# Kernel optimization log

Measured on AMD Instinct MI355X. Metric: run time of the kernel, lower is better.

Reference implementation:

```python
import jax, jax.numpy as jnp
import numpy as np

G = 8          # GroupNorm groups
EPS = 1e-5
L = 4          # num_layers
C = 64         # hidden_channels
CIN = 2        # in_channels


def group_norm(x, gamma, beta):
    B, Cc, H, W = x.shape
    xr = x.reshape(B, G, Cc // G, H, W)
    mu = xr.mean(axis=(2, 3, 4), keepdims=True)
    var = xr.var(axis=(2, 3, 4), keepdims=True)
    xn = ((xr - mu) * jax.lax.rsqrt(var + EPS)).reshape(B, Cc, H, W)
    return xn * gamma[:, None, None] + beta[:, None, None]


def conv1x1(x, w, b):
    # x: [B,Ci,H,W], w: [Co,Ci] -> [B,Co,H,W]
    return jnp.einsum('bchw,oc->bohw', x, w) + b[None, :, None, None]


def conv3x3(x, w, b):
    y = jax.lax.conv_general_dilated(x, w, (1, 1), 'SAME',
                                     dimension_numbers=('NCHW', 'OIHW', 'NCHW'))
    return y + b[None, :, None, None]


def setup_inputs() -> dict:
    key = jax.random.key(0)
    ks = jax.random.split(key, 20)
    s = 0.05
    inp = {
        'x': jax.random.normal(ks[0], (2, CIN, 256, 256), jnp.float32),
        'hidden': jnp.zeros((2, L, C, C), jnp.float32),
        'W_in': jax.random.normal(ks[1], (C, CIN, 3, 3), jnp.float32) * s,
        'b_in': jnp.zeros((C,), jnp.float32),
        'gamma': jnp.ones((L, C), jnp.float32),
        'beta': jnp.zeros((L, C), jnp.float32),
        'Wq': jax.random.normal(ks[2], (L, C, C), jnp.float32) * s,
        'bq': jnp.zeros((L, C), jnp.float32),
        'Wk': jax.random.normal(ks[3], (L, C, C), jnp.float32) * s,
        'bk': jnp.zeros((L, C), jnp.float32),
        'Wv': jax.random.normal(ks[4], (L, C, C), jnp.float32) * s,
        'bv': jnp.zeros((L, C), jnp.float32),
        'Wg': jax.random.normal(ks[5], (L, 2 * C, C), jnp.float32) * s,
        'bg': jnp.zeros((L, 2 * C), jnp.float32),
        'Wp': jax.random.normal(ks[6], (L, C, C), jnp.float32) * s,
        'bp': jnp.zeros((L, C), jnp.float32),
        'W_out': jax.random.normal(ks[7], (CIN, C, 3, 3), jnp.float32) * s,
        'b_out': jnp.zeros((CIN,), jnp.float32),
    }
    return inp


def gla_layer(feat, prev_mem, gamma, beta, Wq, bq, Wk, bk, Wv, bv, Wg, bg, Wp, bp):
    B, Cc, H, W = feat.shape
    N = H * W
    scale = Cc ** (-0.5)
    xn = group_norm(feat, gamma, beta)
    q = conv1x1(xn, Wq, bq).reshape(B, Cc, N) * scale
    k = conv1x1(xn, Wk, bk).reshape(B, Cc, N)
    v = conv1x1(xn, Wv, bv).reshape(B, Cc, N)
    gates = conv1x1(xn, Wg, bg).reshape(B, 2 * Cc, N)
    f_gate = jax.nn.sigmoid(gates[:, :Cc])
    i_gate = jax.nn.sigmoid(gates[:, Cc:])
    k_gated = k * i_gate
    new_knowledge = jnp.einsum('bcn,bdn->bcd', k_gated, v) / N  # [B,C,C]
    global_forget = f_gate.mean(axis=2)[:, :, None]              # [B,C,1]
    new_mem = global_forget * prev_mem + new_knowledge
    retrieved = jnp.einsum('bcn,bcd->bdn', q, new_mem).reshape(B, Cc, H, W)
    out = conv1x1(retrieved, Wp, bp) + feat
    return out, new_mem


def reference(x, hidden, W_in, b_in, gamma, beta, Wq, bq, Wk, bk, Wv, bv,
              Wg, bg, Wp, bp, W_out, b_out):
    feat = conv3x3(x, W_in, b_in)
    mems = []
    for i in range(L):
        feat, m = gla_layer(feat, hidden[:, i], gamma[i], beta[i],
                            Wq[i], bq[i], Wk[i], bk[i], Wv[i], bv[i],
                            Wg[i], bg[i], Wp[i], bp[i])
        mems.append(m)
    new_hidden = jnp.stack(mems, axis=1)  # [B,L,C,C]
    out = conv3x3(feat, W_out, b_out) + x
    return out, new_hidden
```

## Files before the change

kernel.cpp:

```cpp
#include <hip/hip_runtime.h>
#include <hip/hip_bf16.h>

typedef __hip_bfloat16 bf16;
typedef __attribute__((ext_vector_type(8))) short bf16x8;
typedef __attribute__((ext_vector_type(4))) short short4v;
typedef __attribute__((ext_vector_type(4))) float f32x4;

#define BATCH 2
#define CH 64
#define NPIX 65536
#define HDIM 256
#define NLAYER 4
#define NGRP 8

#define OFS_FEAT   0ull
#define OFS_KNOW   33554432ull
#define OFS_FSUM   33685504ull
#define OFS_SSUM   33701888ull
#define OFS_BEFF   33718272ull
#define OFS_MEFFB  33718784ull
#define OFS_WKB    33735168ull
#define OFS_WVB    33767936ull
#define OFS_WGB    33800704ull
#define OFS_WTOUT  33866240ull
#define OFS_WPB    33870848ull
#define OFS_WQTB   33903616ull
#define ZERO_BYTES 163840

__device__ __forceinline__ float sigmoidf_(float x){ return 1.0f/(1.0f+__expf(-x)); }

__device__ __forceinline__ short f2bs(float x){
  unsigned u = __float_as_uint(x);
  u += 0x7fffu + ((u >> 16) & 1u);
  return (short)(u >> 16);
}

__device__ __forceinline__ float waveReduce(float v){
  #pragma unroll
  for (int off=32; off; off>>=1) v += __shfl_xor(v, off, 64);
  return v;
}

__global__ void k_prepw(const float* __restrict__ Wk, const float* __restrict__ Wv,
                        const float* __restrict__ Wg, const float* __restrict__ Wout,
                        const float* __restrict__ Wp, const float* __restrict__ Wq,
                        short* __restrict__ Wkb, short* __restrict__ Wvb,
                        short* __restrict__ Wgb, float* __restrict__ wtout,
                        short* __restrict__ Wpb, short* __restrict__ Wqtb){
  int i = blockIdx.x*256 + threadIdx.x;
  if (i < 16384){
    Wkb[i] = f2bs(Wk[i]);
    Wvb[i] = f2bs(Wv[i]);
    Wpb[i] = f2bs(Wp[i]);
    int l = i >> 12, within = i & 4095;
    int e = within >> 6, c = within & 63;
    Wqtb[i] = f2bs(Wq[l*4096 + c*64 + e]);
  }
  if (i < 32768) Wgb[i] = f2bs(Wg[i]);
  if (i < 1152){
    int o = i / 576, rem = i % 576;
    int k = rem >> 6, c = rem & 63;
    wtout[(o*9 + k)*64 + c] = Wout[o*576 + c*9 + k];
  }
}

__device__ __forceinline__ void blockStats(const float* gs, const float* gq,
                                           float* ssum_b, int t){
  __shared__ float sacc[16];
  if (t < 16) sacc[t] = 0.f;
  __syncthreads();
  #pragma unroll
  for (int g=0; g<NGRP; g++){
    float s  = waveReduce(gs[g]);
    float sq = waveReduce(gq[g]);
    if ((t & 63) == 0){ atomicAdd(&sacc[g*2], s); atomicAdd(&sacc[g*2+1], sq); }
  }
  __syncthreads();
  if (t < 16) atomicAdd(&ssum_b[t*32], sacc[t]);
}

__global__ void k_conv_in(const float* __restrict__ x, const float* __restrict__ w,
                          const float* __restrict__ bias,
                          float* __restrict__ feat, float* __restrict__ ssum){
  int b = blockIdx.y;
  int t = threadIdx.x;
  int n = blockIdx.x*256 + t;
  int y = n >> 8, xx = n & 255;
  float patch[18];
  int idx = 0;
  #pragma unroll
  for (int ci=0; ci<2; ci++)
    #pragma unroll
    for (int dy=-1; dy<=1; dy++)
      #pragma unroll
      for (int dx=-1; dx<=1; dx++){
        int yy = y+dy, xc = xx+dx;
        float v = 0.f;
        if (yy>=0 && yy<HDIM && xc>=0 && xc<HDIM)
          v = x[((b*2+ci)*HDIM + yy)*HDIM + xc];
        patch[idx++] = v;
      }
  float gs[NGRP], gq[NGRP];
  #pragma unroll
  for (int g=0; g<NGRP; g++){ gs[g]=0.f; gq[g]=0.f; }
  float* fb = feat + ((size_t)b*NPIX + n)*64;
  #pragma unroll
  for (int c4=0; c4<16; c4++){
    f32x4 ov;
    #pragma unroll
    for (int j=0;j<4;j++){
      int o = c4*4 + j;
      float acc = bias[o];
      #pragma unroll
      for (int k=0; k<18; k++) acc += w[o*18+k]*patch[k];
      ov[j] = acc;
      gs[o>>3] += acc; gq[o>>3] += acc*acc;
    }
    *(f32x4*)(fb + c4*4) = ov;
  }
  blockStats(gs, gq, ssum + b*512, t);
}

__device__ __forceinline__ void gnCoef(const float* __restrict__ ssum_l, int b, int t,
                                       const float* __restrict__ gammaP,
                                       const float* __restrict__ betaP, int l,
                                       float* s_gnA, float* s_gnB){
  if (t < 64){
    int g = t >> 3;
    const float inv = 1.0f/(8.0f*NPIX);
    float s  = ssum_l[(b*16 + g*2)*32];
    float sq = ssum_l[(b*16 + g*2 + 1)*32];
    float mu = s*inv;
    float var = sq*inv - mu*mu;
    float rstd = rsqrtf(var + 1e-5f);
    float A = rstd * gammaP[l*64 + t];
    s_gnA[t] = A;
    s_gnB[t] = betaP[l*64 + t] - mu * A;
  }
}

__global__ __launch_bounds__(256,3) void k_qkvg_know(
    const float* __restrict__ feat, const float* __restrict__ ssum_l,
    const float* __restrict__ gammaP, const float* __restrict__ betaP,
    const short* __restrict__ Wkb, const float* __restrict__ bkP,
    const short* __restrict__ Wvb, const float* __restrict__ bvP,
    const short* __restrict__ Wgb, const float* __restrict__ bgP,
    int l, float* __restrict__ know, float* __restrict__ f_sum)
{
  int b = blockIdx.y;
  int n0 = blockIdx.x * 128;
  int rep = blockIdx.x & 3;
  int t = threadIdx.x;
  int w = t >> 6;
  int lane = t & 63;
  int m = lane & 15;
  int quad = lane >> 4;
  int rowbase = w*16;

  __shared__ short s_buf[17408];
  short* s_kg = s_buf;
  short* s_v  = s_buf + 8704;
  short* s_xn = s_buf;
  __shared__ float s_gnA[64], s_gnB[64];

  gnCoef(ssum_l, b, t, gammaP, betaP, l, s_gnA, s_gnB);

  float bkv[4], biv[4], bvv[4], bfv[4], fs[4];
  #pragma unroll
  for (int r=0;r<4;r++){
    int row = rowbase + quad*4 + r;
    bkv[r] = bkP[l*64 + row];
    biv[r] = bgP[l*128 + 64 + row];
    bvv[r] = bvP[l*64 + row];
    bfv[r] = bgP[l*128 + row];
    fs[r] = 0.f;
  }
  f32x4 z4 = {0.f,0.f,0.f,0.f};
  f32x4 accn[4];
  #pragma unroll
  for (int dt=0;dt<4;dt++) accn[dt] = z4;

  __syncthreads();

  const float* fbase = feat + ((size_t)b*NPIX + n0)*64;
  #pragma unroll
  for (int i=0;i<8;i++){
    int chunk = t + i*256;
    int px = chunk >> 4, cq = chunk & 15;
    f32x4 fv = *(const f32x4*)(fbase + px*64 + cq*4);
    short4v xs;
    #pragma unroll
    for (int j=0;j<4;j++)
      xs[j] = f2bs(fmaf(fv[j], s_gnA[cq*4+j], s_gnB[cq*4+j]));
    *(short4v*)&s_xn[px*72 + cq*4] = xs;
  }
  __syncthreads();

  bf16x8 Bf[2][8];
  #pragma unroll
  for (int kc=0;kc<2;kc++)
    #pragma unroll
    for (int nt=0;nt<8;nt++)
      Bf[kc][nt] = *(const bf16x8*)&s_xn[(nt*16+m)*72 + kc*32 + quad*8];
  __syncthreads();

  {
    bf16x8 Ak[2], Ai[2];
    #pragma unroll
    for (int kc=0;kc<2;kc++){
      Ak[kc] = *(const bf16x8*)&Wkb[l*4096 + (rowbase+m)*64 + kc*32 + quad*8];
      Ai[kc] = *(const bf16x8*)&Wgb[l*8192 + (64+rowbase+m)*64 + kc*32 + quad*8];
    }
    #pragma unroll
    for (int half=0; half<2; half++){
      f32x4 acck[4], acci[4];
      #pragma unroll
      for (int q4=0;q4<4;q4++){ acck[q4]=z4; acci[q4]=z4; }
      #pragma unroll
      for (int kc=0;kc<2;kc++)
        #pragma unroll
        for (int q4=0;q4<4;q4++){
          acck[q4] = __builtin_amdgcn_mfma_f32_16x16x32_bf16(Ak[kc], Bf[kc][half*4+q4], acck[q4], 0,0,0);
          acci[q4] = __builtin_amdgcn_mfma_f32_16x16x32_bf16(Ai[kc], Bf[kc][half*4+q4], acci[q4], 0,0,0);
        }
      #pragma unroll
      for (int q4=0;q4<4;q4++){
        int nt = half*4+q4;
        #pragma unroll
        for (int r=0;r<4;r++){
          int row = rowbase + quad*4 + r;
          float kv = acck[q4][r] + bkv[r];
          float iv = acci[q4][r] + biv[r];
          s_kg[row*136 + nt*16 + m] = f2bs(kv * sigmoidf_(iv));
        }
      }
    }
  }
  {
    bf16x8 Av[2];
    #pragma unroll
    for (int kc=0;kc<2;kc++)
      Av[kc] = *(const bf16x8*)&Wvb[l*4096 + (rowbase+m)*64 + kc*32 + quad*8];
    #pragma unroll
    for (int half=0; half<2; half++){
      f32x4 accv[4];
      #pragma unroll
      for (int q4=0;q4<4;q4++) accv[q4]=z4;
      #pragma unroll
      for (int kc=0;kc<2;kc++)
        #pragma unroll
        for (int q4=0;q4<4;q4++)
          accv[q4] = __builtin_amdgcn_mfma_f32_16x16x32_bf16(Av[kc], Bf[kc][half*4+q4], accv[q4], 0,0,0);
      #pragma unroll
      for (int q4=0;q4<4;q4++){
        int nt = half*4+q4;
        #pragma unroll
        for (int r=0;r<4;r++){
          int row = rowbase + quad*4 + r;
          s_v[row*136 + nt*16 + m] = f2bs(accv[q4][r] + bvv[r]);
        }
      }
    }
  }
  {
    bf16x8 Af[2];
    #pragma unroll
    for (int kc=0;kc<2;kc++)
      Af[kc] = *(const bf16x8*)&Wgb[l*8192 + (rowbase+m)*64 + kc*32 + quad*8];
    #pragma unroll
    for (int half=0; half<2; half++){
      f32x4 accf[4];
      #pragma unroll
      for (int q4=0;q4<4;q4++) accf[q4]=z4;
      #pragma unroll
      for (int kc=0;kc<2;kc++)
        #pragma unroll
        for (int q4=0;q4<4;q4++)
          accf[q4] = __builtin_amdgcn_mfma_f32_16x16x32_bf16(Af[kc], Bf[kc][half*4+q4], accf[q4], 0,0,0);
      #pragma unroll
      for (int q4=0;q4<4;q4++)
        #pragma unroll
        for (int r=0;r<4;r++)
          fs[r] += sigmoidf_(accf[q4][r] + bfv[r]);
    }
  }
  __syncthreads();

  #pragma unroll
  for (int kc4=0; kc4<4; kc4++){
    bf16x8 a = *(const bf16x8*)&s_kg[(rowbase + m)*136 + kc4*32 + quad*8];
    #pragma unroll
    for (int dt=0; dt<4; dt++){
      bf16x8 bv8 = *(const bf16x8*)&s_v[(dt*16 + m)*136 + kc4*32 + quad*8];
      accn[dt] = __builtin_amdgcn_mfma_f32_16x16x32_bf16(a, bv8, accn[dt], 0,0,0);
    }
  }

  #pragma unroll
  for (int off=1; off<16; off<<=1)
    #pragma unroll
    for (int r=0;r<4;r++) fs[r] += __shfl_xor(fs[r], off, 64);
  if (m == 0){
    #pragma unroll
    for (int r=0;r<4;r++)
      atomicAdd(&f_sum[(b*64 + rowbase + quad*4 + r)*32], fs[r]);
  }
  float* kr = know + (size_t)(rep*2 + b)*4096;
  #pragma unroll
  for (int dt=0;dt<4;dt++)
    #pragma unroll
    for (int r=0;r<4;r++)
      atomicAdd(&kr[(rowbase + quad*4 + r)*64 + dt*16 + m], accn[dt][r]);
}

__global__ __launch_bounds__(256) void k_memupd_meff(
    float* __restrict__ know, float* __restrict__ f_sum,
    const float* __restrict__ hidden_in,
    const short* __restrict__ Wpb, const short* __restrict__ Wqtb,
    const float* __restrict__ bqP, const float* __restrict__ bpP,
    int l, float* __restrict__ hidden_out,
    short* __restrict__ Meffb, float* __restrict__ beff,
    float* __restrict__ ssum_next)
{
  int b = blockIdx.x;
  int t = threadIdx.x;
  int w = t >> 6;
  int lane = t & 63;
  int m = lane & 15;
  int quad = lane >> 4;

  __shared__ short s_memb[64*72];
  __shared__ short s_mfb[64*72];
  __shared__ float s_bq[64];

  if (t < 64) s_bq[t] = bqP[l*64 + t];

  const float invN = 1.0f/(float)NPIX;
  #pragma unroll
  for (int i=0;i<16;i++){
    int cd = t + i*256;
    int c = cd >> 6, d = cd & 63;
    float fmean = f_sum[(b*64 + c)*32] * invN;
    float kn = 0.f;
    #pragma unroll
    for (int rep=0; rep<4; rep++){
      kn += know[(size_t)(rep*2+b)*4096 + cd];
      know[(size_t)(rep*2+b)*4096 + cd] = 0.f;
    }
    kn *= invN;
    float pm = hidden_in[(size_t)(b*NLAYER+l)*4096 + cd];
    float nm = fmean*pm + kn;
    hidden_out[(size_t)(b*NLAYER+l)*4096 + cd] = nm;
    s_memb[c*72 + d] = f2bs(nm);
  }
  __syncthreads();
  if (t < 64) f_sum[(b*64 + t)*32] = 0.f;
  if (t < 16) ssum_next[(b*16 + t)*32] = 0.f;

  f32x4 z4 = {0.f,0.f,0.f,0.f};

  bf16x8 Ap[2];
  #pragma unroll
  for (int kc=0;kc<2;kc++)
    Ap[kc] = *(const bf16x8*)&Wpb[l*4096 + (w*16+m)*64 + kc*32 + quad*8];

  float be[4];
  #pragma unroll
  for (int r=0;r<4;r++) be[r] = 0.f;

  #pragma unroll
  for (int ct=0; ct<4; ct++){
    f32x4 a = z4;
    #pragma unroll
    for (int kc=0;kc<2;kc++){
      bf16x8 Bm = *(const bf16x8*)&s_memb[(ct*16+m)*72 + kc*32 + quad*8];
      a = __builtin_amdgcn_mfma_f32_16x16x32_bf16(Ap[kc], Bm, a, 0,0,0);
    }
    int c = ct*16 + m;
    #pragma unroll
    for (int r=0;r<4;r++){
      int o = w*16 + quad*4 + r;
      s_mfb[o*72 + c] = f2bs(a[r]);
      be[r] += a[r] * s_bq[c];
    }
  }
  #pragma unroll
  for (int off=1; off<16; off<<=1)
    #pragma unroll
    for (int r=0;r<4;r++) be[r] += __shfl_xor(be[r], off, 64);
  if (m == 0){
    #pragma unroll
    for (int r=0;r<4;r++){
      int o = w*16 + quad*4 + r;
      beff[b*64 + o] = bpP[l*64 + o] + 0.125f*be[r];
    }
  }
  __syncthreads();

  bf16x8 Am2[2];
  #pragma unroll
  for (int kc=0;kc<2;kc++)
    Am2[kc] = *(const bf16x8*)&s_mfb[(w*16+m)*72 + kc*32 + quad*8];
  #pragma unroll
  for (int et=0; et<4; et++){
    f32x4 a = z4;
    #pragma unroll
    for (int kc=0;kc<2;kc++){
      bf16x8 Bq = *(const bf16x8*)&Wqtb[l*4096 + (et*16+m)*64 + kc*32 + quad*8];
      a = __builtin_amdgcn_mfma_f32_16x16x32_bf16(Am2[kc], Bq, a, 0,0,0);
    }
    #pragma unroll
    for (int r=0;r<4;r++){
      int o = w*16 + quad*4 + r;
      Meffb[(size_t)b*4096 + o*64 + et*16 + m] = f2bs(0.125f*a[r]);
    }
  }
}

__global__ __launch_bounds__(256,3) void k_retrproj(
    const float* __restrict__ ssum_l,
    const float* __restrict__ gammaP, const float* __restrict__ betaP,
    const short* __restrict__ Meffb, const float* __restrict__ beff,
    int l, float* __restrict__ feat, float* __restrict__ ssum_next)
{
  int b = blockIdx.y;
  int n0 = blockIdx.x * 128;
  int t = threadIdx.x;
  int w = t >> 6;
  int lane = t & 63;
  int m = lane & 15;
  int quad = lane >> 4;

  __shared__ float s_out[128*68];
  short* s_xn = (short*)s_out;
  __shared__ float s_gnA[64], s_gnB[64], s_beff[64];
  __shared__ float s_sacc[16];

  gnCoef(ssum_l, b, t, gammaP, betaP, l, s_gnA, s_gnB);
  if (t < 64) s_beff[t] = beff[b*64 + t];
  if (t < 16) s_sacc[t] = 0.f;
  __syncthreads();

  const float* fbase = feat + ((size_t)b*NPIX + n0)*64;
  #pragma unroll
  for (int i=0;i<8;i++){
    int chunk = t + i*256;
    int px = chunk >> 4, cq = chunk & 15;
    f32x4 fv = *(const f32x4*)(fbase + px*64 + cq*4);
    short4v xs;
    #pragma unroll
    for (int j=0;j<4;j++)
      xs[j] = f2bs(fmaf(fv[j], s_gnA[cq*4+j], s_gnB[cq*4+j]));
    *(short4v*)&s_xn[px*72 + cq*4] = xs;
  }
  __syncthreads();

  bf16x8 Bf[2][8];
  #pragma unroll
  for (int kc=0;kc<2;kc++)
    #pragma unroll
    for (int nt=0;nt<8;nt++)
      Bf[kc][nt] = *(const bf16x8*)&s_xn[(nt*16+m)*72 + kc*32 + quad*8];

  bf16x8 Am[2];
  #pragma unroll
  for (int kc=0;kc<2;kc++)
    Am[kc] = *(const bf16x8*)&Meffb[(size_t)b*4096 + (w*16 + m)*64 + kc*32 + quad*8];
  __syncthreads();

  f32x4 acc[8];
  f32x4 z4 = {0.f,0.f,0.f,0.f};
  #pragma unroll
  for (int nt=0;nt<8;nt++) acc[nt]=z4;
  #pragma unroll
  for (int kc=0;kc<2;kc++)
    #pragma unroll
    for (int nt=0;nt<8;nt++)
      acc[nt] = __builtin_amdgcn_mfma_f32_16x16x32_bf16(Am[kc], Bf[kc][nt], acc[nt], 0,0,0);

  #pragma unroll
  for (int nt=0;nt<8;nt++)
    #pragma unroll
    for (int r=0;r<4;r++)
      s_out[(nt*16+m)*68 + w*16 + quad*4 + r] = acc[nt][r];
  __syncthreads();

  float gsv = 0.f, gqv = 0.f;
  int cq = t & 15;
  #pragma unroll
  for (int i=0;i<8;i++){
    int chunk = t + i*256;
    int px = chunk >> 4;
    float* fp = (float*)(fbase + px*64 + cq*4);
    f32x4 fv = *(const f32x4*)fp;
    f32x4 ov = *(const f32x4*)&s_out[px*68 + cq*4];
    f32x4 res;
    #pragma unroll
    for (int j=0;j<4;j++){
      float o = fv[j] + ov[j] + s_beff[cq*4+j];
      res[j] = o;
      gsv += o; gqv += o*o;
    }
    *(f32x4*)fp = res;
  }
  gsv += __shfl_xor(gsv, 1, 64);  gqv += __shfl_xor(gqv, 1, 64);
  gsv += __shfl_xor(gsv, 16, 64); gqv += __shfl_xor(gqv, 16, 64);
  gsv += __shfl_xor(gsv, 32, 64); gqv += __shfl_xor(gqv, 32, 64);
  if ((lane & 49) == 0){
    int g = (lane & 15) >> 1;
    atomicAdd(&s_sacc[g*2], gsv);
    atomicAdd(&s_sacc[g*2+1], gqv);
  }
  __syncthreads();
  if (t < 16) atomicAdd(&ssum_next[(b*16 + t)*32], s_sacc[t]);
}

__global__ void k_conv_out(const float* __restrict__ feat, const float* __restrict__ wt,
                           const float* __restrict__ bias,
                           const float* __restrict__ xin, float* __restrict__ out){
  int b = blockIdx.y;
  int y = blockIdx.x;
  int xx = threadIdx.x;
  float acc0 = bias[0], acc1 = bias[1];
  #pragma unroll
  for (int dy=-1; dy<=1; dy++){
    int yy = y + dy;
    if (yy < 0 || yy >= HDIM) continue;
    #pragma unroll
    for (int dx=-1; dx<=1; dx++){
      int xc = xx + dx;
      if (xc >= 0 && xc < HDIM){
        const float* fp = feat + ((size_t)b*NPIX + yy*HDIM + xc)*64;
        const float* w0 = wt + ((0*3 + dy+1)*3 + dx+1)*64;
        const float* w1 = wt + ((1*3 + dy+1)*3 + dx+1)*64;
        #pragma unroll
        for (int c4=0;c4<16;c4++){
          f32x4 fv  = *(const f32x4*)(fp + c4*4);
          f32x4 wv0 = *(const f32x4*)(w0 + c4*4);
          f32x4 wv1 = *(const f32x4*)(w1 + c4*4);
          #pragma unroll
          for (int j=0;j<4;j++){
            acc0 += fv[j]*wv0[j];
            acc1 += fv[j]*wv1[j];
          }
        }
      }
    }
  }
  size_t p0 = (size_t)(b*2+0)*NPIX + y*HDIM + xx;
  size_t p1 = (size_t)(b*2+1)*NPIX + y*HDIM + xx;
  out[p0] = acc0 + xin[p0];
  out[p1] = acc1 + xin[p1];
}

extern "C" void kernel_launch(void* const* d_in, const int* in_sizes, int n_in,
                              void* d_out, int out_size, void* d_ws, size_t ws_size,
                              hipStream_t stream){
  char* ws = (char*)d_ws;
  float* feat  = (float*)(ws + OFS_FEAT);
  float* know  = (float*)(ws + OFS_KNOW);
  float* fsum  = (float*)(ws + OFS_FSUM);
  float* ssum  = (float*)(ws + OFS_SSUM);
  float* beff  = (float*)(ws + OFS_BEFF);
  short* meffb = (short*)(ws + OFS_MEFFB);
  short* wkb   = (short*)(ws + OFS_WKB);
  short* wvb   = (short*)(ws + OFS_WVB);
  short* wgb   = (short*)(ws + OFS_WGB);
  float* wtout = (float*)(ws + OFS_WTOUT);
  short* wpb   = (short*)(ws + OFS_WPB);
  short* wqtb  = (short*)(ws + OFS_WQTB);

  const float* x      = (const float*)d_in[0];
  const float* hidden = (const float*)d_in[1];
  const float* W_in   = (const float*)d_in[2];
  const float* b_in   = (const float*)d_in[3];
  const float* gamma  = (const float*)d_in[4];
  const float* beta   = (const float*)d_in[5];
  const float* Wq     = (const float*)d_in[6];
  const float* bq     = (const float*)d_in[7];
  const float* Wk     = (const float*)d_in[8];
  const float* bk     = (const float*)d_in[9];
  const float* Wv     = (const float*)d_in[10];
  const float* bv     = (const float*)d_in[11];
  const float* Wg     = (const float*)d_in[12];
  const float* bg     = (const float*)d_in[13];
  const float* Wp     = (const float*)d_in[14];
  const float* bp     = (const float*)d_in[15];
  const float* W_out  = (const float*)d_in[16];
  const float* b_out  = (const float*)d_in[17];

  float* out        = (float*)d_out;
  float* hidden_out = out + BATCH*2*NPIX;

  hipMemsetAsync(ws + OFS_KNOW, 0, ZERO_BYTES, stream);
  k_prepw<<<dim3(128), dim3(256), 0, stream>>>(Wk, Wv, Wg, W_out, Wp, Wq,
                                               wkb, wvb, wgb, wtout, wpb, wqtb);
  k_conv_in<<<dim3(HDIM, BATCH), dim3(256), 0, stream>>>(x, W_in, b_in, feat, ssum);

  for (int l=0; l<NLAYER; l++){
    float* ssum_l = ssum + (l & 1)*1024;
    float* ssum_n = ssum + ((l+1) & 1)*1024;
    k_qkvg_know<<<dim3(NPIX/128, BATCH), dim3(256), 0, stream>>>(
        feat, ssum_l, gamma, beta, wkb, bk, wvb, bv, wgb, bg, l, know, fsum);
    k_memupd_meff<<<dim3(BATCH), dim3(256), 0, stream>>>(
        know, fsum, hidden, wpb, wqtb, bq, bp, l, hidden_out, meffb, beff, ssum_n);
    k_retrproj<<<dim3(NPIX/128, BATCH), dim3(256), 0, stream>>>(
        ssum_l, gamma, beta, meffb, beff, l, feat, ssum_n);
  }

  k_conv_out<<<dim3(HDIM, BATCH), dim3(256), 0, stream>>>(feat, wtout, b_out, x, out);
}
```

Before: 404.3 us.

## Factor V projection out of knowledge accumulation and register-stage feat loads

```diff
diff --git a/kernel.cpp b/kernel.cpp
--- a/kernel.cpp
+++ b/kernel.cpp
@@ -14,18 +14,19 @@
 #define NGRP 8
 
 #define OFS_FEAT   0ull
-#define OFS_KNOW   33554432ull
+#define OFS_KX     33554432ull
 #define OFS_FSUM   33685504ull
-#define OFS_SSUM   33701888ull
-#define OFS_BEFF   33718272ull
-#define OFS_MEFFB  33718784ull
-#define OFS_WKB    33735168ull
-#define OFS_WVB    33767936ull
-#define OFS_WGB    33800704ull
-#define OFS_WTOUT  33866240ull
-#define OFS_WPB    33870848ull
-#define OFS_WQTB   33903616ull
-#define ZERO_BYTES 163840
+#define OFS_KGS    33701888ull
+#define OFS_SSUM   33718272ull
+#define OFS_BEFF   33734656ull
+#define OFS_MEFFB  33735168ull
+#define OFS_WKB    33751552ull
+#define OFS_WVB    33784320ull
+#define OFS_WGB    33817088ull
+#define OFS_WTOUT  33882624ull
+#define OFS_WPB    33887232ull
+#define OFS_WQTB   33920000ull
+#define ZERO_BYTES 180224
 
 __device__ __forceinline__ float sigmoidf_(float x){ return 1.0f/(1.0f+__expf(-x)); }
 
@@ -143,9 +144,9 @@
     const float* __restrict__ feat, const float* __restrict__ ssum_l,
     const float* __restrict__ gammaP, const float* __restrict__ betaP,
     const short* __restrict__ Wkb, const float* __restrict__ bkP,
-    const short* __restrict__ Wvb, const float* __restrict__ bvP,
     const short* __restrict__ Wgb, const float* __restrict__ bgP,
-    int l, float* __restrict__ know, float* __restrict__ f_sum)
+    int l, float* __restrict__ kx, float* __restrict__ f_sum,
+    float* __restrict__ kg_sum)
 {
   int b = blockIdx.y;
   int n0 = blockIdx.x * 128;
@@ -157,42 +158,46 @@
   int quad = lane >> 4;
   int rowbase = w*16;
 
-  __shared__ short s_buf[17408];
-  short* s_kg = s_buf;
-  short* s_v  = s_buf + 8704;
-  short* s_xn = s_buf;
+  __shared__ short s_xn[128*72];
+  __shared__ short s_xnT[64*136];
   __shared__ float s_gnA[64], s_gnB[64];
+  short* s_kg = s_xn;
+
+  const float* fbase = feat + ((size_t)b*NPIX + n0)*64;
+  f32x4 fv[8];
+  #pragma unroll
+  for (int i=0;i<8;i++){
+    int chunk = t + i*256;
+    fv[i] = *(const f32x4*)(fbase + (chunk >> 4)*64 + (chunk & 15)*4);
+  }
 
   gnCoef(ssum_l, b, t, gammaP, betaP, l, s_gnA, s_gnB);
 
-  float bkv[4], biv[4], bvv[4], bfv[4], fs[4];
+  float bkv[4], biv[4], bfv[4], fs[4], kgs[4];
   #pragma unroll
   for (int r=0;r<4;r++){
     int row = rowbase + quad*4 + r;
     bkv[r] = bkP[l*64 + row];
     biv[r] = bgP[l*128 + 64 + row];
-    bvv[r] = bvP[l*64 + row];
     bfv[r] = bgP[l*128 + row];
-    fs[r] = 0.f;
+    fs[r] = 0.f; kgs[r] = 0.f;
   }
   f32x4 z4 = {0.f,0.f,0.f,0.f};
-  f32x4 accn[4];
-  #pragma unroll
-  for (int dt=0;dt<4;dt++) accn[dt] = z4;
-
-  __syncthreads();
-
-  const float* fbase = feat + ((size_t)b*NPIX + n0)*64;
+
+  __syncthreads();
+
   #pragma unroll
   for (int i=0;i<8;i++){
     int chunk = t + i*256;
-    int px = chunk >> 4, cq = chunk & 15;
-    f32x4 fv = *(const f32x4*)(fbase + px*64 + cq*4);
+    int px = chunk >> 4, c0 = (chunk & 15)*4;
     short4v xs;
     #pragma unroll
     for (int j=0;j<4;j++)
-      xs[j] = f2bs(fmaf(fv[j], s_gnA[cq*4+j], s_gnB[cq*4+j]));
-    *(short4v*)&s_xn[px*72 + cq*4] = xs;
+      xs[j] = f2bs(fmaf(fv[i][j], s_gnA[c0+j], s_gnB[c0+j]));
+    *(short4v*)&s_xn[px*72 + c0] = xs;
+    #pragma unroll
+    for (int j=0;j<4;j++)
+      s_xnT[(c0+j)*136 + px] = xs[j];
   }
   __syncthreads();
 
@@ -231,33 +236,9 @@
           int row = rowbase + quad*4 + r;
           float kv = acck[q4][r] + bkv[r];
           float iv = acci[q4][r] + biv[r];
-          s_kg[row*136 + nt*16 + m] = f2bs(kv * sigmoidf_(iv));
-        }
-      }
-    }
-  }
-  {
-    bf16x8 Av[2];
-    #pragma unroll
-    for (int kc=0;kc<2;kc++)
-      Av[kc] = *(const bf16x8*)&Wvb[l*4096 + (rowbase+m)*64 + kc*32 + quad*8];
-    #pragma unroll
-    for (int half=0; half<2; half++){
-      f32x4 accv[4];
-      #pragma unroll
-      for (int q4=0;q4<4;q4++) accv[q4]=z4;
-      #pragma unroll
-      for (int kc=0;kc<2;kc++)
-        #pragma unroll
-        for (int q4=0;q4<4;q4++)
-          accv[q4] = __builtin_amdgcn_mfma_f32_16x16x32_bf16(Av[kc], Bf[kc][half*4+q4], accv[q4], 0,0,0);
-      #pragma unroll
-      for (int q4=0;q4<4;q4++){
-        int nt = half*4+q4;
-        #pragma unroll
-        for (int r=0;r<4;r++){
-          int row = rowbase + quad*4 + r;
-          s_v[row*136 + nt*16 + m] = f2bs(accv[q4][r] + bvv[r]);
+          float kgv = kv * sigmoidf_(iv);
+          s_kg[row*136 + nt*16 + m] = f2bs(kgv);
+          kgs[r] += kgv;
         }
       }
     }
@@ -284,28 +265,36 @@
           fs[r] += sigmoidf_(accf[q4][r] + bfv[r]);
     }
   }
-  __syncthreads();
-
+
+  f32x4 accn[4];
+  #pragma unroll
+  for (int dt=0;dt<4;dt++) accn[dt] = z4;
   #pragma unroll
   for (int kc4=0; kc4<4; kc4++){
     bf16x8 a = *(const bf16x8*)&s_kg[(rowbase + m)*136 + kc4*32 + quad*8];
     #pragma unroll
     for (int dt=0; dt<4; dt++){
-      bf16x8 bv8 = *(const bf16x8*)&s_v[(dt*16 + m)*136 + kc4*32 + quad*8];
-      accn[dt] = __builtin_amdgcn_mfma_f32_16x16x32_bf16(a, bv8, accn[dt], 0,0,0);
+      bf16x8 bx = *(const bf16x8*)&s_xnT[(dt*16 + m)*136 + kc4*32 + quad*8];
+      accn[dt] = __builtin_amdgcn_mfma_f32_16x16x32_bf16(a, bx, accn[dt], 0,0,0);
     }
   }
 
   #pragma unroll
   for (int off=1; off<16; off<<=1)
     #pragma unroll
-    for (int r=0;r<4;r++) fs[r] += __shfl_xor(fs[r], off, 64);
+    for (int r=0;r<4;r++){
+      fs[r]  += __shfl_xor(fs[r],  off, 64);
+      kgs[r] += __shfl_xor(kgs[r], off, 64);
+    }
   if (m == 0){
     #pragma unroll
-    for (int r=0;r<4;r++)
-      atomicAdd(&f_sum[(b*64 + rowbase + quad*4 + r)*32], fs[r]);
-  }
-  float* kr = know + (size_t)(rep*2 + b)*4096;
+    for (int r=0;r<4;r++){
+      int row = rowbase + quad*4 + r;
+      atomicAdd(&f_sum[(b*64 + row)*32], fs[r]);
+      atomicAdd(&kg_sum[(b*64 + row)*32], kgs[r]);
+    }
+  }
+  float* kr = kx + (size_t)(rep*2 + b)*4096;
   #pragma unroll
   for (int dt=0;dt<4;dt++)
     #pragma unroll
@@ -314,8 +303,9 @@
 }
 
 __global__ __launch_bounds__(256) void k_memupd_meff(
-    float* __restrict__ know, float* __restrict__ f_sum,
+    float* __restrict__ kx, float* __restrict__ f_sum, float* __restrict__ kg_sum,
     const float* __restrict__ hidden_in,
+    const short* __restrict__ Wvb, const float* __restrict__ bvP,
     const short* __restrict__ Wpb, const short* __restrict__ Wqtb,
     const float* __restrict__ bqP, const float* __restrict__ bpP,
     int l, float* __restrict__ hidden_out,
@@ -328,46 +318,72 @@
   int lane = t & 63;
   int m = lane & 15;
   int quad = lane >> 4;
-
+  const float invN = 1.0f/(float)NPIX;
+
+  __shared__ short s_kxb[64*72];
   __shared__ short s_memb[64*72];
   __shared__ short s_mfb[64*72];
-  __shared__ float s_bq[64];
-
-  if (t < 64) s_bq[t] = bqP[l*64 + t];
-
-  const float invN = 1.0f/(float)NPIX;
+  __shared__ float s_bq[64], s_bv[64], s_fm[64], s_kgs[64];
+
+  if (t < 64){
+    s_bq[t]  = bqP[l*64 + t];
+    s_bv[t]  = bvP[l*64 + t];
+    s_fm[t]  = f_sum[(b*64 + t)*32] * invN;
+    s_kgs[t] = kg_sum[(b*64 + t)*32] * invN;
+  }
   #pragma unroll
   for (int i=0;i<16;i++){
-    int cd = t + i*256;
-    int c = cd >> 6, d = cd & 63;
-    float fmean = f_sum[(b*64 + c)*32] * invN;
-    float kn = 0.f;
+    int ce = t + i*256;
+    float s = 0.f;
     #pragma unroll
     for (int rep=0; rep<4; rep++){
-      kn += know[(size_t)(rep*2+b)*4096 + cd];
-      know[(size_t)(rep*2+b)*4096 + cd] = 0.f;
-    }
-    kn *= invN;
-    float pm = hidden_in[(size_t)(b*NLAYER+l)*4096 + cd];
-    float nm = fmean*pm + kn;
-    hidden_out[(size_t)(b*NLAYER+l)*4096 + cd] = nm;
-    s_memb[c*72 + d] = f2bs(nm);
-  }
-  __syncthreads();
-  if (t < 64) f_sum[(b*64 + t)*32] = 0.f;
-  if (t < 16) ssum_next[(b*16 + t)*32] = 0.f;
+      s += kx[(size_t)(rep*2+b)*4096 + ce];
+      kx[(size_t)(rep*2+b)*4096 + ce] = 0.f;
+    }
+    s_kxb[(ce>>6)*72 + (ce&63)] = f2bs(s);
+  }
+  __syncthreads();
+  if (t < 64){ f_sum[(b*64+t)*32] = 0.f; kg_sum[(b*64+t)*32] = 0.f; }
+  if (t < 16) ssum_next[(b*16+t)*32] = 0.f;
 
   f32x4 z4 = {0.f,0.f,0.f,0.f};
+
+  bf16x8 Akx[2];
+  #pragma unroll
+  for (int kc=0;kc<2;kc++)
+    Akx[kc] = *(const bf16x8*)&s_kxb[(w*16+m)*72 + kc*32 + quad*8];
+  float pm[4][4];
+  #pragma unroll
+  for (int ct=0; ct<4; ct++)
+    #pragma unroll
+    for (int r=0;r<4;r++)
+      pm[ct][r] = hidden_in[(size_t)(b*NLAYER+l)*4096 + (w*16+quad*4+r)*64 + ct*16+m];
+  #pragma unroll
+  for (int ct=0; ct<4; ct++){
+    f32x4 a = z4;
+    #pragma unroll
+    for (int kc=0;kc<2;kc++){
+      bf16x8 Bv = *(const bf16x8*)&Wvb[l*4096 + (ct*16+m)*64 + kc*32 + quad*8];
+      a = __builtin_amdgcn_mfma_f32_16x16x32_bf16(Akx[kc], Bv, a, 0,0,0);
+    }
+    #pragma unroll
+    for (int r=0;r<4;r++){
+      int c = w*16 + quad*4 + r;
+      int d = ct*16 + m;
+      float nm = s_fm[c]*pm[ct][r] + a[r]*invN + s_kgs[c]*s_bv[d];
+      hidden_out[(size_t)(b*NLAYER+l)*4096 + c*64 + d] = nm;
+      s_memb[c*72 + d] = f2bs(nm);
+    }
+  }
+  __syncthreads();
 
   bf16x8 Ap[2];
   #pragma unroll
   for (int kc=0;kc<2;kc++)
     Ap[kc] = *(const bf16x8*)&Wpb[l*4096 + (w*16+m)*64 + kc*32 + quad*8];
-
   float be[4];
   #pragma unroll
   for (int r=0;r<4;r++) be[r] = 0.f;
-
   #pragma unroll
   for (int ct=0; ct<4; ct++){
     f32x4 a = z4;
@@ -431,27 +447,36 @@
   int m = lane & 15;
   int quad = lane >> 4;
 
-  __shared__ float s_out[128*68];
-  short* s_xn = (short*)s_out;
+  __shared__ short s_xn[128*72];
   __shared__ float s_gnA[64], s_gnB[64], s_beff[64];
   __shared__ float s_sacc[16];
+
+  const float* fbase = feat + ((size_t)b*NPIX + n0)*64;
+  f32x4 fv[8];
+  #pragma unroll
+  for (int i=0;i<8;i++){
+    int chunk = t + i*256;
+    fv[i] = *(const f32x4*)(fbase + (chunk >> 4)*64 + (chunk & 15)*4);
+  }
+  bf16x8 Am[2];
+  #pragma unroll
+  for (int kc=0;kc<2;kc++)
+    Am[kc] = *(const bf16x8*)&Meffb[(size_t)b*4096 + (w*16 + m)*64 + kc*32 + quad*8];
 
   gnCoef(ssum_l, b, t, gammaP, betaP, l, s_gnA, s_gnB);
   if (t < 64) s_beff[t] = beff[b*64 + t];
   if (t < 16) s_sacc[t] = 0.f;
   __syncthreads();
 
-  const float* fbase = feat + ((size_t)b*NPIX + n0)*64;
   #pragma unroll
   for (int i=0;i<8;i++){
     int chunk = t + i*256;
-    int px = chunk >> 4, cq = chunk & 15;
-    f32x4 fv = *(const f32x4*)(fbase + px*64 + cq*4);
+    int px = chunk >> 4, c0 = (chunk & 15)*4;
     short4v xs;
     #pragma unroll
     for (int j=0;j<4;j++)
-      xs[j] = f2bs(fmaf(fv[j], s_gnA[cq*4+j], s_gnB[cq*4+j]));
-    *(short4v*)&s_xn[px*72 + cq*4] = xs;
+      xs[j] = f2bs(fmaf(fv[i][j], s_gnA[c0+j], s_gnB[c0+j]));
+    *(short4v*)&s_xn[px*72 + c0] = xs;
   }
   __syncthreads();
 
@@ -462,12 +487,6 @@
     for (int nt=0;nt<8;nt++)
       Bf[kc][nt] = *(const bf16x8*)&s_xn[(nt*16+m)*72 + kc*32 + quad*8];
 
-  bf16x8 Am[2];
-  #pragma unroll
-  for (int kc=0;kc<2;kc++)
-    Am[kc] = *(const bf16x8*)&Meffb[(size_t)b*4096 + (w*16 + m)*64 + kc*32 + quad*8];
-  __syncthreads();
-
   f32x4 acc[8];
   f32x4 z4 = {0.f,0.f,0.f,0.f};
   #pragma unroll
@@ -478,36 +497,30 @@
     for (int nt=0;nt<8;nt++)
       acc[nt] = __builtin_amdgcn_mfma_f32_16x16x32_bf16(Am[kc], Bf[kc][nt], acc[nt], 0,0,0);
 
-  #pragma unroll
-  for (int nt=0;nt<8;nt++)
-    #pragma unroll
-    for (int r=0;r<4;r++)
-      s_out[(nt*16+m)*68 + w*16 + quad*4 + r] = acc[nt][r];
-  __syncthreads();
-
+  int c0 = w*16 + quad*4;
+  f32x4 bev = *(const f32x4*)&s_beff[c0];
   float gsv = 0.f, gqv = 0.f;
-  int cq = t & 15;
-  #pragma unroll
-  for (int i=0;i<8;i++){
-    int chunk = t + i*256;
-    int px = chunk >> 4;
-    float* fp = (float*)(fbase + px*64 + cq*4);
-    f32x4 fv = *(const f32x4*)fp;
-    f32x4 ov = *(const f32x4*)&s_out[px*68 + cq*4];
+  #pragma unroll
+  for (int nt=0;nt<8;nt++){
+    int px = nt*16 + m;
+    float* fp = (float*)(fbase + px*64 + c0);
+    f32x4 old = *(const f32x4*)fp;
     f32x4 res;
     #pragma unroll
     for (int j=0;j<4;j++){
-      float o = fv[j] + ov[j] + s_beff[cq*4+j];
+      float o = old[j] + acc[nt][j] + bev[j];
       res[j] = o;
       gsv += o; gqv += o*o;
     }
     *(f32x4*)fp = res;
   }
-  gsv += __shfl_xor(gsv, 1, 64);  gqv += __shfl_xor(gqv, 1, 64);
-  gsv += __shfl_xor(gsv, 16, 64); gqv += __shfl_xor(gqv, 16, 64);
-  gsv += __shfl_xor(gsv, 32, 64); gqv += __shfl_xor(gqv, 32, 64);
-  if ((lane & 49) == 0){
-    int g = (lane & 15) >> 1;
+  #pragma unroll
+  for (int off=1; off<32; off<<=1){
+    gsv += __shfl_xor(gsv, off, 64);
+    gqv += __shfl_xor(gqv, off, 64);
+  }
+  if ((lane & 31) == 0){
+    int g = 2*w + (lane >> 5);
     atomicAdd(&s_sacc[g*2], gsv);
     atomicAdd(&s_sacc[g*2+1], gqv);
   }
@@ -535,13 +548,13 @@
         const float* w1 = wt + ((1*3 + dy+1)*3 + dx+1)*64;
         #pragma unroll
         for (int c4=0;c4<16;c4++){
-          f32x4 fv  = *(const f32x4*)(fp + c4*4);
+          f32x4 fvv = *(const f32x4*)(fp + c4*4);
           f32x4 wv0 = *(const f32x4*)(w0 + c4*4);
           f32x4 wv1 = *(const f32x4*)(w1 + c4*4);
           #pragma unroll
           for (int j=0;j<4;j++){
-            acc0 += fv[j]*wv0[j];
-            acc1 += fv[j]*wv1[j];
+            acc0 += fvv[j]*wv0[j];
+            acc1 += fvv[j]*wv1[j];
           }
         }
       }
@@ -558,8 +571,9 @@
                               hipStream_t stream){
   char* ws = (char*)d_ws;
   float* feat  = (float*)(ws + OFS_FEAT);
-  float* know  = (float*)(ws + OFS_KNOW);
+  float* kxb   = (float*)(ws + OFS_KX);
   float* fsum  = (float*)(ws + OFS_FSUM);
+  float* kgs   = (float*)(ws + OFS_KGS);
   float* ssum  = (float*)(ws + OFS_SSUM);
   float* beff  = (float*)(ws + OFS_BEFF);
   short* meffb = (short*)(ws + OFS_MEFFB);
@@ -592,7 +606,7 @@
   float* out        = (float*)d_out;
   float* hidden_out = out + BATCH*2*NPIX;
 
-  hipMemsetAsync(ws + OFS_KNOW, 0, ZERO_BYTES, stream);
+  hipMemsetAsync(ws + OFS_KX, 0, ZERO_BYTES, stream);
   k_prepw<<<dim3(128), dim3(256), 0, stream>>>(Wk, Wv, Wg, W_out, Wp, Wq,
                                                wkb, wvb, wgb, wtout, wpb, wqtb);
   k_conv_in<<<dim3(HDIM, BATCH), dim3(256), 0, stream>>>(x, W_in, b_in, feat, ssum);
@@ -601,9 +615,10 @@
     float* ssum_l = ssum + (l & 1)*1024;
     float* ssum_n = ssum + ((l+1) & 1)*1024;
     k_qkvg_know<<<dim3(NPIX/128, BATCH), dim3(256), 0, stream>>>(
-        feat, ssum_l, gamma, beta, wkb, bk, wvb, bv, wgb, bg, l, know, fsum);
+        feat, ssum_l, gamma, beta, wkb, bk, wgb, bg, l, kxb, fsum, kgs);
     k_memupd_meff<<<dim3(BATCH), dim3(256), 0, stream>>>(
-        know, fsum, hidden, wpb, wqtb, bq, bp, l, hidden_out, meffb, beff, ssum_n);
+        kxb, fsum, kgs, hidden, wvb, bv, wpb, wqtb, bq, bp, l, hidden_out,
+        meffb, beff, ssum_n);
     k_retrproj<<<dim3(NPIX/128, BATCH), dim3(256), 0, stream>>>(
         ssum_l, gamma, beta, meffb, beff, l, feat, ssum_n);
   }
```

Result: slower. 445.6 us (+10.2%).
